# Performance work log

Hardware: AMD Instinct MI355X
Metric: run time of the kernel (lower is better)

The kernel has to match this reference:

```python
import jax, jax.numpy as jnp
import numpy as np

# NSA hyperparams (match init_kwargs)
D_BLK = 64    # d: block stride
L_CMP = 64    # compression block length (== d -> non-overlapping blocks)
L_SLC = 64    # selection block length (== l_cmp == d -> P_slc = P_cmp)
BQ = 64       # block_size_q
TOPK = 16     # slc_top_k
WL, WR = 512, 0  # sliding window (left, right)


def _nsa_forward(q, k, v, w_k, b_k, w_v, b_v, w_gate, b_gate, seqlen):
    S, qh, dim = q.shape
    kv = k.shape[1]
    H = qh // kv
    b = S // seqlen          # number of equal-length packed sequences
    s = seqlen
    scale = dim ** -0.5
    f32 = jnp.float32

    # [b, s, kv, H, e]: q head g*H+h belongs to kv head g (repeat_interleave layout)
    q5 = q.reshape(b, s, kv, H, dim)
    k3 = k.reshape(b, s, kv, dim)
    v3 = v.reshape(b, s, kv, dim)

    # ---- block compression (extract_blocks + cmp_linear over block length) ----
    n_blk = s // D_BLK
    kb = k.reshape(b, n_blk, D_BLK, kv, dim)
    vb = v.reshape(b, n_blk, D_BLK, kv, dim)
    K_cmp = jnp.einsum('bntke,t->bnke', kb, w_k) + b_k[0]
    V_cmp = jnp.einsum('bntke,t->bnke', vb, w_v) + b_v[0]

    # ---- compressed attention (per sequence, fp32 softmax) ----
    sc = jnp.einsum('bqkhe,bnke->bkhqn', q5, K_cmp).astype(f32) * scale
    P = jax.nn.softmax(sc, axis=-1)
    out_cmp = jnp.einsum('bkhqn,bnke->bqkhe', P.astype(q.dtype), V_cmp)

    # ---- selection scores: pool P over q-blocks and GQA groups, then top-k ----
    nqb = s // BQ
    pooled = P.reshape(b, kv, H, nqb, BQ, n_blk).sum(axis=(2, 4))  # [b,kv,nqb,n_blk]
    idx = jax.lax.top_k(pooled, TOPK)[1]                            # [b,kv,nqb,TOPK]

    # gather selected K/V blocks (shared by all queries in a q-block / GQA group)
    kb2 = jnp.transpose(kb, (0, 3, 1, 2, 4))  # [b,kv,n_blk,l,e]
    vb2 = jnp.transpose(vb, (0, 3, 1, 2, 4))
    gather = jax.vmap(jax.vmap(lambda blocks, i: blocks[i]))
    K_sel = gather(kb2, idx)  # [b,kv,nqb,TOPK,l,e]
    V_sel = gather(vb2, idx)

    # ---- selected-block attention ----
    qblk = q5.reshape(b, nqb, BQ, kv, H, dim)
    sc2 = jnp.einsum('bnckhe,bkntle->bkhnctl', qblk, K_sel).astype(f32) * scale
    sc2 = sc2.reshape(b, kv, H, nqb, BQ, TOPK * L_SLC)
    P2 = jax.nn.softmax(sc2, axis=-1).astype(q.dtype)
    out_slc = jnp.einsum('bkhncm,bknme->bnckhe', P2,
                         V_sel.reshape(b, kv, nqb, TOPK * L_SLC, dim))
    out_slc = out_slc.reshape(b, s, kv, H, dim)

    # ---- sliding-window attention (window_size=(WL, WR), non-causal flag) ----
    sw = jnp.einsum('bikhe,bjke->bkhij', q5, k3).astype(f32) * scale
    i = jnp.arange(s)[:, None]
    j = jnp.arange(s)[None, :]
    valid = (j >= i - WL) & (j <= i + WR)
    sw = jnp.where(valid, sw, -jnp.inf)
    Pw = jax.nn.softmax(sw, axis=-1).astype(q.dtype)
    out_win = jnp.einsum('bkhij,bjke->bikhe', Pw, v3)

    # ---- gated fusion of the three branches ----
    gate = jax.nn.sigmoid(jnp.einsum('bqkhe,ec->bqkhc', q5, w_gate) + b_gate)
    out = (gate[..., 0:1] * out_cmp
           + gate[..., 1:2] * out_slc
           + gate[..., 2:3] * out_win)
    return out.reshape(S, qh, dim)


def setup_inputs() -> dict:
    key = jax.random.key(0)
    ks = jax.random.split(key, 9)
    S, qh, kvh, dim = 4096, 8, 2, 128
    inp = {
        'q': jax.random.normal(ks[0], (S, qh, dim), jnp.float32),
        'k': jax.random.normal(ks[1], (S, kvh, dim), jnp.float32),
        'v': jax.random.normal(ks[2], (S, kvh, dim), jnp.float32),
        'w_k': jax.random.normal(ks[3], (L_CMP,), jnp.float32) * (L_CMP ** -0.5),
        'b_k': jax.random.normal(ks[4], (1,), jnp.float32) * 0.02,
        'w_v': jax.random.normal(ks[5], (L_CMP,), jnp.float32) * (L_CMP ** -0.5),
        'b_v': jax.random.normal(ks[6], (1,), jnp.float32) * 0.02,
        'w_gate': jax.random.normal(ks[7], (dim, 3), jnp.float32) * (dim ** -0.5),
        'b_gate': jax.random.normal(ks[8], (3,), jnp.float32) * 0.02,
        'seqlen': 2048,
    }
    return inp


def reference(q, k, v, w_k, b_k, w_v, b_v, w_gate, b_gate, seqlen):
    return _nsa_forward(q, k, v, w_k, b_k, w_v, b_v, w_gate, b_gate, seqlen)
```

## Files before the change

kernel.cpp:

```cpp
#include <hip/hip_runtime.h>
#include <hip/hip_bf16.h>


#define SEQ   2048
#define NB    2
#define KV    2
#define NH    4
#define QH    8
#define DIM   128
#define NBLK  32
#define NQB   32
#define NTOP  16
#define SCALE 0.08838834764831845f
#define QSC   0.12751831795244785f
#define VP    72
#define VCS   40

typedef unsigned short ushort_t;
using bf16x8 = __attribute__((ext_vector_type(8))) short;
using f32x4  = __attribute__((ext_vector_type(4))) float;

__device__ __forceinline__ unsigned pkbf(float a, float b){
  union { __hip_bfloat162 h; unsigned u; } cv;
  cv.h = __float22bfloat162_rn(make_float2(a, b));
  return cv.u;
}
__device__ __forceinline__ ushort_t b16(float f){
  union { float f; unsigned i; } x; x.f = f;
  unsigned r = x.i + 0x7fffu + ((x.i >> 16) & 1u);
  return (ushort_t)(r >> 16);
}
__device__ __forceinline__ float fb(ushort_t h){
  union { unsigned i; float f; } x; x.i = ((unsigned)h) << 16;
  return x.f;
}

__device__ __forceinline__ void async16(ushort_t* l, const ushort_t* g){
  __builtin_amdgcn_global_load_lds(
      (const __attribute__((address_space(1))) unsigned int*)(size_t)g,
      (__attribute__((address_space(3))) unsigned int*)(size_t)l,
      16, 0, 0);
}

__global__ __launch_bounds__(256) void prep_k(
    const float* __restrict__ k, const float* __restrict__ v,
    const float* __restrict__ w_k, const float* __restrict__ b_k,
    const float* __restrict__ w_v, const float* __restrict__ b_v,
    ushort_t* __restrict__ Kb, ushort_t* __restrict__ VT,
    float* __restrict__ Kc, float* __restrict__ Vc)
{
  int blk = blockIdx.x;
  int db = blk & 1, rb = (blk >> 1) & 31, bbg = blk >> 6;
  int bb = bbg >> 1, g = bbg & 1;
  int tid = threadIdx.x;
  __shared__ ushort_t T[64*VP];
  __shared__ float wks[64], wvs[64];
  __shared__ float accK[16][64], accV[16][64];

  if (tid < 64){ wks[tid] = w_k[tid]; wvs[tid] = w_v[tid]; }
  __syncthreads();

  float4 sk = {0,0,0,0}, sv = {0,0,0,0};
  for (int jj = 0; jj < 4; ++jj){
    int i = tid + jj*256;
    int r = i >> 4, ds = i & 15;
    size_t src = ((size_t)(bb*SEQ + rb*64 + r)*KV + g)*DIM + db*64 + ds*4;
    float4 kx = *(const float4*)(k + src);
    float4 vx = *(const float4*)(v + src);
    uint2 kk; kk.x = pkbf(kx.x,kx.y); kk.y = pkbf(kx.z,kx.w);
    size_t rowb = ((size_t)bbg*SEQ + rb*64 + r)*DIM*2;
    int swz = (db*128 + ds*8) ^ ((r & 7) << 4);
    *(uint2*)((char*)Kb + rowb + swz) = kk;
    unsigned v01 = pkbf(vx.x,vx.y), v23 = pkbf(vx.z,vx.w);
    T[(ds*4+0)*VP + r] = (ushort_t)(v01 & 0xffffu);
    T[(ds*4+1)*VP + r] = (ushort_t)(v01 >> 16);
    T[(ds*4+2)*VP + r] = (ushort_t)(v23 & 0xffffu);
    T[(ds*4+3)*VP + r] = (ushort_t)(v23 >> 16);
    float a = wks[r], b = wvs[r];
    sk.x += a*kx.x; sk.y += a*kx.y; sk.z += a*kx.z; sk.w += a*kx.w;
    sv.x += b*vx.x; sv.y += b*vx.y; sv.z += b*vx.z; sv.w += b*vx.w;
  }
  *(float4*)&accK[tid>>4][(tid&15)*4] = sk;
  *(float4*)&accV[tid>>4][(tid&15)*4] = sv;
  __syncthreads();

  for (int jj = 0; jj < 4; ++jj){
    int i = tid + jj*256;
    int d = i >> 4, seg = i & 15;
    uint2 u = *(uint2*)&T[d*VP + seg*4];
    size_t rowb = ((size_t)bbg*DIM + db*64 + d)*SEQ*2;
    int swz = (seg*8) ^ ((d & 7) << 4);
    *(uint2*)((char*)VT + rowb + rb*128 + swz) = u;
  }

  size_t obase = ((size_t)(bbg*NBLK + rb))*DIM + db*64;
  if (tid < 64){
    float s = 0.f;
#pragma unroll
    for (int i = 0; i < 16; ++i) s += accK[i][tid];
    Kc[obase + tid] = s + b_k[0];
  } else if (tid < 128){
    int d = tid - 64;
    float s = 0.f;
#pragma unroll
    for (int i = 0; i < 16; ++i) s += accV[i][d];
    Vc[obase + d] = s + b_v[0];
  }
}

__global__ __launch_bounds__(512, 2) void attn_k(
    const float* __restrict__ q, const ushort_t* __restrict__ Kb,
    const ushort_t* __restrict__ VT,
    const float* __restrict__ Kc, const float* __restrict__ Vc,
    const float* __restrict__ w_gate, const float* __restrict__ b_gate,
    float* __restrict__ slcbuf, float* __restrict__ out)
{
  int idx = blockIdx.x;
  int x = idx & 7, low = idx & 1, u = idx >> 3;
  int bbg = x >> 1;
  int j = u*2 + low;
  int role = j >> 5;
  int qb = j & 31;
  int bb = bbg >> 1, g = bbg & 1;

  int tid = threadIdx.x;
  int lane = tid & 63, w = tid >> 6;
  int quad = lane >> 4, l15 = lane & 15;
  int h = w & 3, qh2 = w >> 2;
  int xr = (l15 & 7) << 4;

  __shared__ ushort_t Ks[2][64*128];
  __shared__ ushort_t VTs[3][128*64];
  __shared__ ushort_t Ps[256*VP];
  __shared__ ushort_t VcTh[128*VCS];
  __shared__ ushort_t VcTl[128*VCS];
  __shared__ float pw[8][NBLK];
  __shared__ float gbuf[256];
  __shared__ int   idxs[NTOP];

  if (role == 0){
    {
      int key = tid >> 4, dq = tid & 15;
      const float* kcs = Kc + ((size_t)bbg*NBLK + key)*DIM + dq*8;
      float4 f0 = *(const float4*)kcs, f1 = *(const float4*)(kcs + 4);
      float fe[8] = {f0.x,f0.y,f0.z,f0.w,f1.x,f1.y,f1.z,f1.w};
      union { ushort_t u[8]; uint4 v; } hi, lo;
#pragma unroll
      for (int e = 0; e < 8; ++e){
        ushort_t hh = b16(fe[e]);
        hi.u[e] = hh; lo.u[e] = b16(fe[e] - fb(hh));
      }
      int off = (dq*16) ^ ((key & 7) << 4);
      *(uint4*)((char*)&Ks[0][0] + key*256 + off) = hi.v;
      *(uint4*)((char*)&Ks[0][0] + (key+32)*256 + off) = lo.v;
    }
    {
      int d = tid & 127, kq = tid >> 7;
      const float* vcs = Vc + (size_t)bbg*NBLK*DIM + d;
      union { ushort_t u[8]; uint4 v; } hi, lo;
#pragma unroll
      for (int kk = 0; kk < 8; ++kk){
        float f = vcs[(kq*8 + kk)*DIM];
        ushort_t hh = b16(f);
        hi.u[kk] = hh; lo.u[kk] = b16(f - fb(hh));
      }
      *(uint4*)&VcTh[d*VCS + kq*8] = hi.v;
      *(uint4*)&VcTl[d*VCS + kq*8] = lo.v;
    }
  }

  const float* qrow0 = q + ((size_t)(bb*SEQ + qb*64 + qh2*32 + l15)*QH + g*NH + h)*DIM;
  const float* qrow1 = qrow0 + (size_t)16*QH*DIM;
  int gcol = 1 + role;
  bf16x8 qfrag0[4], qfrag1[4], qlo0[4], qlo1[4];
  float gp0 = 0.f, gp1 = 0.f, gc0 = 0.f, gc1 = 0.f;
#pragma unroll
  for (int kc = 0; kc < 4; ++kc){
    int d0 = kc*32 + quad*8;
    float4 a0 = *(const float4*)(qrow0 + d0);
    float4 a1 = *(const float4*)(qrow0 + d0 + 4);
    float4 b0 = *(const float4*)(qrow1 + d0);
    float4 b1 = *(const float4*)(qrow1 + d0 + 4);
    float qa[8] = {a0.x,a0.y,a0.z,a0.w,a1.x,a1.y,a1.z,a1.w};
    float qc[8] = {b0.x,b0.y,b0.z,b0.w,b1.x,b1.y,b1.z,b1.w};
#pragma unroll
    for (int jj = 0; jj < 8; ++jj){
      float wg = w_gate[(d0+jj)*3 + gcol];
      gp0 += qa[jj]*wg; gp1 += qc[jj]*wg;
    }
    if (role == 0){
#pragma unroll
      for (int jj = 0; jj < 8; ++jj){
        float w0 = w_gate[(d0+jj)*3];
        gc0 += qa[jj]*w0; gc1 += qc[jj]*w0;
      }
      union { ushort_t u[8]; bf16x8 v; } h0, l0, h1, l1;
#pragma unroll
      for (int e = 0; e < 8; ++e){
        float s0f = qa[e]*QSC; ushort_t hh0 = b16(s0f);
        h0.u[e] = hh0; l0.u[e] = b16(s0f - fb(hh0));
        float s1f = qc[e]*QSC; ushort_t hh1 = b16(s1f);
        h1.u[e] = hh1; l1.u[e] = b16(s1f - fb(hh1));
      }
      qfrag0[kc] = h0.v; qlo0[kc] = l0.v;
      qfrag1[kc] = h1.v; qlo1[kc] = l1.v;
    } else {
      union { unsigned uu[4]; bf16x8 v8; } t0, t1;
#pragma unroll
      for (int p2 = 0; p2 < 4; ++p2){
        t0.uu[p2] = pkbf(qa[2*p2]*QSC, qa[2*p2+1]*QSC);
        t1.uu[p2] = pkbf(qc[2*p2]*QSC, qc[2*p2+1]*QSC);
      }
      qfrag0[kc] = t0.v8; qfrag1[kc] = t1.v8;
    }
  }
  gp0 += __shfl_xor(gp0,16); gp0 += __shfl_xor(gp0,32);
  gp1 += __shfl_xor(gp1,16); gp1 += __shfl_xor(gp1,32);
  if (quad == 0){
    gbuf[w*32 + l15]      = 1.f/(1.f + __expf(-(gp0 + b_gate[gcol])));
    gbuf[w*32 + 16 + l15] = 1.f/(1.f + __expf(-(gp1 + b_gate[gcol])));
  }
  float g0c0 = 0.f, g0c1 = 0.f;
  if (role == 0){
    gc0 += __shfl_xor(gc0,16); gc0 += __shfl_xor(gc0,32);
    gc1 += __shfl_xor(gc1,16); gc1 += __shfl_xor(gc1,32);
    g0c0 = 1.f/(1.f + __expf(-(gc0 + b_gate[0])));
    g0c1 = 1.f/(1.f + __expf(-(gc1 + b_gate[0])));
  }
  __syncthreads();
  float gl0[4], gl1[4];
#pragma unroll
  for (int r = 0; r < 4; ++r){
    gl0[r] = gbuf[w*32 + quad*4 + r];
    gl1[r] = gbuf[w*32 + 16 + quad*4 + r];
  }

  const f32x4 zero4 = {0.f,0.f,0.f,0.f};
  f32x4 cp0[2], cp1[2];
  cp0[0] = zero4; cp0[1] = zero4; cp1[0] = zero4; cp1[1] = zero4;

  if (role == 0){
    f32x4 c0[2], c1[2];
    c0[0]=zero4; c0[1]=zero4; c1[0]=zero4; c1[1]=zero4;
#pragma unroll
    for (int kc = 0; kc < 4; ++kc){
#pragma unroll
      for (int nt = 0; nt < 2; ++nt){
        bf16x8 ah = *(bf16x8*)((char*)&Ks[0][0] + (nt*16 + l15)*256
                               + ((kc*64 + quad*16) ^ xr));
        bf16x8 al = *(bf16x8*)((char*)&Ks[0][0] + (nt*16 + l15 + 32)*256
                               + ((kc*64 + quad*16) ^ xr));
        c0[nt] = __builtin_amdgcn_mfma_f32_16x16x32_bf16(ah, qfrag0[kc], c0[nt], 0, 0, 0);
        c0[nt] = __builtin_amdgcn_mfma_f32_16x16x32_bf16(ah, qlo0[kc],   c0[nt], 0, 0, 0);
        c0[nt] = __builtin_amdgcn_mfma_f32_16x16x32_bf16(al, qfrag0[kc], c0[nt], 0, 0, 0);
        c1[nt] = __builtin_amdgcn_mfma_f32_16x16x32_bf16(ah, qfrag1[kc], c1[nt], 0, 0, 0);
        c1[nt] = __builtin_amdgcn_mfma_f32_16x16x32_bf16(ah, qlo1[kc],   c1[nt], 0, 0, 0);
        c1[nt] = __builtin_amdgcn_mfma_f32_16x16x32_bf16(al, qfrag1[kc], c1[nt], 0, 0, 0);
      }
    }
    float mx0 = -INFINITY, mx1 = -INFINITY;
#pragma unroll
    for (int nt = 0; nt < 2; ++nt)
#pragma unroll
      for (int r = 0; r < 4; ++r){
        mx0 = fmaxf(mx0, c0[nt][r]); mx1 = fmaxf(mx1, c1[nt][r]);
      }
    mx0 = fmaxf(mx0, __shfl_xor(mx0,16)); mx0 = fmaxf(mx0, __shfl_xor(mx0,32));
    mx1 = fmaxf(mx1, __shfl_xor(mx1,16)); mx1 = fmaxf(mx1, __shfl_xor(mx1,32));
    float s0 = 0.f, s1 = 0.f;
#pragma unroll
    for (int nt = 0; nt < 2; ++nt)
#pragma unroll
      for (int r = 0; r < 4; ++r){
        float p0v = exp2f(c0[nt][r] - mx0); c0[nt][r] = p0v; s0 += p0v;
        float p1v = exp2f(c1[nt][r] - mx1); c1[nt][r] = p1v; s1 += p1v;
      }
    s0 += __shfl_xor(s0,16); s0 += __shfl_xor(s0,32);
    s1 += __shfl_xor(s1,16); s1 += __shfl_xor(s1,32);
    float ip0 = 1.f/s0, ip1 = 1.f/s1;
    float ig0 = g0c0*ip0, ig1 = g0c1*ip1;
#pragma unroll
    for (int nt = 0; nt < 2; ++nt)
#pragma unroll
      for (int r = 0; r < 4; ++r){
        cp0[nt][r] = c0[nt][r]*ig0;
        cp1[nt][r] = c1[nt][r]*ig1;
        float t = c0[nt][r]*ip0 + c1[nt][r]*ip1;
        t += __shfl_xor(t,1); t += __shfl_xor(t,2);
        t += __shfl_xor(t,4); t += __shfl_xor(t,8);
        if (l15 == 0) pw[w][nt*16 + quad*4 + r] = t;
      }
    __syncthreads();
    if (tid < 64){
      int n = lane;
      float val = -INFINITY;
      if (n < NBLK){
        float sm = 0.f;
#pragma unroll
        for (int w2 = 0; w2 < 8; ++w2) sm += pw[w2][n];
        val = sm;
      }
      int idxv = n;
      for (int kk = 2; kk <= 32; kk <<= 1){
        for (int jj2 = kk >> 1; jj2 > 0; jj2 >>= 1){
          float pv = __shfl_xor(val, jj2);
          int   pi = __shfl_xor(idxv, jj2);
          bool lower = (lane & jj2) == 0;
          bool desc  = (lane & kk) == 0;
          bool iwin  = (val > pv) || (val == pv && idxv < pi);
          bool keep  = (lower == desc) ? iwin : !iwin;
          if (!keep){ val = pv; idxv = pi; }
        }
      }
      if (lane < NTOP) idxs[lane] = idxv;
    }
    __syncthreads();
  }

  const ushort_t* kbase  = Kb + (size_t)bbg*SEQ*DIM;
  const ushort_t* vtbase = VT + (size_t)bbg*DIM*SEQ;

  int kb0 = (qb >= 8) ? (qb - 8) : 0;
  int nph = (role == 0) ? NTOP : (qb - kb0 + 1);
  int qi0 = qh2*32 + l15, qi1 = qi0 + 16;

  float m10 = -INFINITY, l10 = 0.f, m11 = -INFINITY, l11 = 0.f;
  f32x4 oacc0[8], oacc1[8];
#pragma unroll
  for (int dt = 0; dt < 8; ++dt){ oacc0[dt] = zero4; oacc1[dt] = zero4; }

  auto stage = [&](int kbuf, int vbuf, int kb_){
    const ushort_t* ksrc = kbase + (size_t)kb_*64*DIM;
#pragma unroll
    for (int jj = 0; jj < 2; ++jj)
      async16(&Ks[kbuf][(jj*512 + w*64)*8], ksrc + (size_t)(tid + jj*512)*8);
    const ushort_t* vsrc = vtbase + kb_*64;
#pragma unroll
    for (int jj = 0; jj < 2; ++jj){
      int i = tid + jj*512;
      int d = i >> 3, sg = i & 7;
      async16(&VTs[vbuf][(jj*512 + w*64)*8], vsrc + (size_t)d*SEQ + sg*8);
    }
  };

  stage(0, 0, (role == 0) ? idxs[0] : kb0);

  float alp0 = 1.f, alp1 = 1.f;
  bool  skp0 = true,  skp1 = true;
  int vprev = 2, vcur = 0, vnext = 1;

  for (int t = 0; t < nph; ++t){
    int kb = (role == 0) ? idxs[t] : (kb0 + t);
    __syncthreads();
    if (t+1 < nph){
      int kbn = (role == 0) ? idxs[t+1] : (kb0 + t + 1);
      stage((t+1) & 1, vnext, kbn);
    }
    __builtin_amdgcn_sched_barrier(0);

    f32x4 sacc0[4], sacc1[4];
#pragma unroll
    for (int nt = 0; nt < 4; ++nt){ sacc0[nt] = zero4; sacc1[nt] = zero4; }
    __builtin_amdgcn_s_setprio(1);
#pragma unroll
    for (int kc = 0; kc < 4; ++kc){
#pragma unroll
      for (int nt = 0; nt < 4; ++nt){
        bf16x8 a = *(bf16x8*)((char*)&Ks[t & 1][0] + (nt*16 + l15)*256
                              + ((kc*64 + quad*16) ^ xr));
        sacc0[nt] = __builtin_amdgcn_mfma_f32_16x16x32_bf16(a, qfrag0[kc], sacc0[nt], 0, 0, 0);
        sacc1[nt] = __builtin_amdgcn_mfma_f32_16x16x32_bf16(a, qfrag1[kc], sacc1[nt], 0, 0, 0);
      }
    }
    __builtin_amdgcn_s_setprio(0);

    if (t > 0){
      if (!skp0){
        float ar[4];
#pragma unroll
        for (int r = 0; r < 4; ++r) ar[r] = __shfl(alp0, quad*4 + r);
#pragma unroll
        for (int dt = 0; dt < 8; ++dt)
#pragma unroll
          for (int r = 0; r < 4; ++r) oacc0[dt][r] *= ar[r];
      }
      if (!skp1){
        float ar[4];
#pragma unroll
        for (int r = 0; r < 4; ++r) ar[r] = __shfl(alp1, quad*4 + r);
#pragma unroll
        for (int dt = 0; dt < 8; ++dt)
#pragma unroll
          for (int r = 0; r < 4; ++r) oacc1[dt][r] *= ar[r];
      }
#pragma unroll
      for (int kc2 = 0; kc2 < 2; ++kc2){
        bf16x8 pa0 = *(bf16x8*)&Ps[(w*32 + l15)*VP + kc2*32 + quad*8];
        bf16x8 pa1 = *(bf16x8*)&Ps[(w*32 + 16 + l15)*VP + kc2*32 + quad*8];
        __builtin_amdgcn_s_setprio(1);
#pragma unroll
        for (int dt = 0; dt < 8; ++dt){
          bf16x8 vb8 = *(bf16x8*)((char*)&VTs[vprev][0] + (dt*16 + l15)*128
                                  + ((kc2*64 + quad*16) ^ xr));
          oacc0[dt] = __builtin_amdgcn_mfma_f32_16x16x32_bf16(pa0, vb8, oacc0[dt], 0, 0, 0);
          oacc1[dt] = __builtin_amdgcn_mfma_f32_16x16x32_bf16(pa1, vb8, oacc1[dt], 0, 0, 0);
        }
        __builtin_amdgcn_s_setprio(0);
      }
    }

    bool mlow  = (role == 1) && (kb == qb - 8);
    bool mhigh = (role == 1) && (kb == qb);
    bool domask = mlow | mhigh;

    auto softmax_qt = [&](f32x4* sc2, float& m1r, float& l1r, int qi_l,
                          bool& skipped) -> float {
      if (domask){
#pragma unroll
        for (int nt = 0; nt < 4; ++nt)
#pragma unroll
          for (int r = 0; r < 4; ++r){
            int key = nt*16 + quad*4 + r;
            bool valid = (!mlow || key >= qi_l) && (!mhigh || key <= qi_l);
            sc2[nt][r] = valid ? sc2[nt][r] : -INFINITY;
          }
      }
      float mnt[4];
#pragma unroll
      for (int nt = 0; nt < 4; ++nt)
        mnt[nt] = fmaxf(fmaxf(sc2[nt][0], sc2[nt][1]),
                        fmaxf(sc2[nt][2], sc2[nt][3]));
      float mx = fmaxf(fmaxf(mnt[0], mnt[1]), fmaxf(mnt[2], mnt[3]));
      mx = fmaxf(mx, __shfl_xor(mx, 16));
      mx = fmaxf(mx, __shfl_xor(mx, 32));
      float al = 1.f;
      skipped = __all(mx <= m1r + 8.f);
      if (!skipped){
        float mn = fmaxf(m1r, mx);
        al = exp2f(m1r - mn);
        m1r = mn;
      }
      float snt[4];
#pragma unroll
      for (int nt = 0; nt < 4; ++nt){
        float p0 = exp2f(sc2[nt][0] - m1r);
        float p1 = exp2f(sc2[nt][1] - m1r);
        float p2 = exp2f(sc2[nt][2] - m1r);
        float p3 = exp2f(sc2[nt][3] - m1r);
        sc2[nt][0] = p0; sc2[nt][1] = p1; sc2[nt][2] = p2; sc2[nt][3] = p3;
        snt[nt] = (p0 + p1) + (p2 + p3);
      }
      float s0 = (snt[0] + snt[1]) + (snt[2] + snt[3]);
      s0 += __shfl_xor(s0, 16);
      s0 += __shfl_xor(s0, 32);
      l1r = l1r*al + s0;
      return al;
    };
    bool sk0, sk1;
    float al0 = softmax_qt(sacc0, m10, l10, qi0, sk0);
    float al1 = softmax_qt(sacc1, m11, l11, qi1, sk1);
    alp0 = al0; skp0 = sk0;
    alp1 = al1; skp1 = sk1;

#pragma unroll
    for (int nt = 0; nt < 4; ++nt){
      uint2 p0, p1;
      p0.x = pkbf(sacc0[nt][0], sacc0[nt][1]);
      p0.y = pkbf(sacc0[nt][2], sacc0[nt][3]);
      p1.x = pkbf(sacc1[nt][0], sacc1[nt][1]);
      p1.y = pkbf(sacc1[nt][2], sacc1[nt][3]);
      *(uint2*)&Ps[(w*32 + l15)*VP + nt*16 + quad*4] = p0;
      *(uint2*)&Ps[(w*32 + 16 + l15)*VP + nt*16 + quad*4] = p1;
    }

    int tmpv = vprev; vprev = vcur; vcur = vnext; vnext = tmpv;
  }

  {
    if (!skp0){
      float ar[4];
#pragma unroll
      for (int r = 0; r < 4; ++r) ar[r] = __shfl(alp0, quad*4 + r);
#pragma unroll
      for (int dt = 0; dt < 8; ++dt)
#pragma unroll
        for (int r = 0; r < 4; ++r) oacc0[dt][r] *= ar[r];
    }
    if (!skp1){
      float ar[4];
#pragma unroll
      for (int r = 0; r < 4; ++r) ar[r] = __shfl(alp1, quad*4 + r);
#pragma unroll
      for (int dt = 0; dt < 8; ++dt)
#pragma unroll
        for (int r = 0; r < 4; ++r) oacc1[dt][r] *= ar[r];
    }
#pragma unroll
    for (int kc2 = 0; kc2 < 2; ++kc2){
      bf16x8 pa0 = *(bf16x8*)&Ps[(w*32 + l15)*VP + kc2*32 + quad*8];
      bf16x8 pa1 = *(bf16x8*)&Ps[(w*32 + 16 + l15)*VP + kc2*32 + quad*8];
#pragma unroll
      for (int dt = 0; dt < 8; ++dt){
        bf16x8 vb8 = *(bf16x8*)((char*)&VTs[vprev][0] + (dt*16 + l15)*128
                                + ((kc2*64 + quad*16) ^ xr));
        oacc0[dt] = __builtin_amdgcn_mfma_f32_16x16x32_bf16(pa0, vb8, oacc0[dt], 0, 0, 0);
        oacc1[dt] = __builtin_amdgcn_mfma_f32_16x16x32_bf16(pa1, vb8, oacc1[dt], 0, 0, 0);
      }
    }
  }

  float lr0[4], lr1[4];
#pragma unroll
  for (int r = 0; r < 4; ++r){
    lr0[r] = __shfl(l10, quad*4 + r);
    lr1[r] = __shfl(l11, quad*4 + r);
  }
  if (role == 0){
    float a0[4], a1[4];
#pragma unroll
    for (int r = 0; r < 4; ++r){ a0[r] = gl0[r]/lr0[r]; a1[r] = gl1[r]/lr1[r]; }
#pragma unroll
    for (int dt = 0; dt < 8; ++dt)
#pragma unroll
      for (int r = 0; r < 4; ++r){ oacc0[dt][r] *= a0[r]; oacc1[dt][r] *= a1[r]; }
#pragma unroll
    for (int nt = 0; nt < 2; ++nt){
      union { ushort_t u[4]; uint2 v; } h0, l0, h1, l1;
#pragma unroll
      for (int r = 0; r < 4; ++r){
        ushort_t hh0 = b16(cp0[nt][r]);
        h0.u[r] = hh0; l0.u[r] = b16(cp0[nt][r] - fb(hh0));
        ushort_t hh1 = b16(cp1[nt][r]);
        h1.u[r] = hh1; l1.u[r] = b16(cp1[nt][r] - fb(hh1));
      }
      *(uint2*)&Ps[(w*32 + l15)*VP + nt*16 + quad*4]      = h0.v;
      *(uint2*)&Ps[(w*32 + l15)*VP + 32 + nt*16 + quad*4] = l0.v;
      *(uint2*)&Ps[(w*32 + 16 + l15)*VP + nt*16 + quad*4]      = h1.v;
      *(uint2*)&Ps[(w*32 + 16 + l15)*VP + 32 + nt*16 + quad*4] = l1.v;
    }
    bf16x8 pah0 = *(bf16x8*)&Ps[(w*32 + l15)*VP + quad*8];
    bf16x8 pal0 = *(bf16x8*)&Ps[(w*32 + l15)*VP + 32 + quad*8];
    bf16x8 pah1 = *(bf16x8*)&Ps[(w*32 + 16 + l15)*VP + quad*8];
    bf16x8 pal1 = *(bf16x8*)&Ps[(w*32 + 16 + l15)*VP + 32 + quad*8];
#pragma unroll
    for (int dt = 0; dt < 8; ++dt){
      bf16x8 vbh = *(bf16x8*)&VcTh[(dt*16 + l15)*VCS + quad*8];
      bf16x8 vbl = *(bf16x8*)&VcTl[(dt*16 + l15)*VCS + quad*8];
      oacc0[dt] = __builtin_amdgcn_mfma_f32_16x16x32_bf16(pah0, vbh, oacc0[dt], 0, 0, 0);
      oacc0[dt] = __builtin_amdgcn_mfma_f32_16x16x32_bf16(pah0, vbl, oacc0[dt], 0, 0, 0);
      oacc0[dt] = __builtin_amdgcn_mfma_f32_16x16x32_bf16(pal0, vbh, oacc0[dt], 0, 0, 0);
      oacc1[dt] = __builtin_amdgcn_mfma_f32_16x16x32_bf16(pah1, vbh, oacc1[dt], 0, 0, 0);
      oacc1[dt] = __builtin_amdgcn_mfma_f32_16x16x32_bf16(pah1, vbl, oacc1[dt], 0, 0, 0);
      oacc1[dt] = __builtin_amdgcn_mfma_f32_16x16x32_bf16(pal1, vbh, oacc1[dt], 0, 0, 0);
    }
#pragma unroll
    for (int r = 0; r < 4; ++r){
      size_t ob0 = ((size_t)(bb*SEQ + qb*64 + qh2*32 + quad*4 + r)*QH + g*NH + h)*DIM + l15;
      size_t ob1 = ob0 + (size_t)16*QH*DIM;
      float* op0 = slcbuf + ob0;
      float* op1 = slcbuf + ob1;
#pragma unroll
      for (int dt = 0; dt < 8; ++dt){
        op0[dt*16] = oacc0[dt][r];
        op1[dt*16] = oacc1[dt][r];
      }
    }
  } else {
#pragma unroll
    for (int r = 0; r < 4; ++r){
      float s20 = gl0[r] / lr0[r];
      float s21 = gl1[r] / lr1[r];
      size_t ob0 = ((size_t)(bb*SEQ + qb*64 + qh2*32 + quad*4 + r)*QH + g*NH + h)*DIM + l15;
      size_t ob1 = ob0 + (size_t)16*QH*DIM;
      float* op0 = out + ob0;
      float* op1 = out + ob1;
#pragma unroll
      for (int dt = 0; dt < 8; ++dt){
        op0[dt*16] = s20 * oacc0[dt][r];
        op1[dt*16] = s21 * oacc1[dt][r];
      }
    }
  }
}

__global__ __launch_bounds__(256) void merge_k(const float* __restrict__ slcbuf,
                                               float* __restrict__ out){
  int i = blockIdx.x * 256 + threadIdx.x;
  float4 a = ((const float4*)slcbuf)[i];
  float4 b = ((float4*)out)[i];
  b.x += a.x; b.y += a.y; b.z += a.z; b.w += a.w;
  ((float4*)out)[i] = b;
}

extern "C" void kernel_launch(void* const* d_in, const int* in_sizes, int n_in,
                              void* d_out, int out_size, void* d_ws, size_t ws_size,
                              hipStream_t stream) {
  const float* q      = (const float*)d_in[0];
  const float* k      = (const float*)d_in[1];
  const float* v      = (const float*)d_in[2];
  const float* w_k    = (const float*)d_in[3];
  const float* b_k    = (const float*)d_in[4];
  const float* w_v    = (const float*)d_in[5];
  const float* b_v    = (const float*)d_in[6];
  const float* w_gate = (const float*)d_in[7];
  const float* b_gate = (const float*)d_in[8];
  float* out = (float*)d_out;

  float* ws     = (float*)d_ws;
  float* Kc     = ws;
  float* Vc     = ws + 16384;
  float* slcbuf = ws + 49152;
  ushort_t* Kb  = (ushort_t*)(ws + 4243456);
  ushort_t* VT  = Kb + 1048576;

  prep_k <<<256, 256, 0, stream>>>(k, v, w_k, b_k, w_v, b_v, Kb, VT, Kc, Vc);
  attn_k <<<256, 512, 0, stream>>>(q, Kb, VT, Kc, Vc, w_gate, b_gate, slcbuf, out);
  merge_k<<<4096, 256, 0, stream>>>(slcbuf, out);
}
```

Measured before the change: 162.9 us.

## Split KV range across two blocks per tile with split-softmax merge

Doubles the attn grid so each selection and sliding-window tile is handled by two blocks, each covering half of the KV blocks. Partial outputs go out unnormalized along with per-row max and sum, and the merge kernel combines them flash-decoding style. The compressed-attention P·V product moves out of the attention kernel into the merge kernel as an fp32 loop over 32 compressed values. Async LDS double/triple buffering is replaced by register-staged single-buffer loads with extra barriers, which shrinks LDS so occupancy can rise to 4 blocks per CU. The cost is more global traffic through the new device buffers and less overlap of loads with compute.

```diff
diff --git a/kernel.cpp b/kernel.cpp
--- a/kernel.cpp
+++ b/kernel.cpp
@@ -14,11 +14,16 @@
 #define SCALE 0.08838834764831845f
 #define QSC   0.12751831795244785f
 #define VP    72
-#define VCS   40
+#define VSU   68
 
 typedef unsigned short ushort_t;
 using bf16x8 = __attribute__((ext_vector_type(8))) short;
 using f32x4  = __attribute__((ext_vector_type(4))) float;
+
+__device__ float g_slcB[4194304];
+__device__ float g_winB[4194304];
+__device__ float g_cp[1048576];
+__device__ float g_mlg[4][65536];
 
 __device__ __forceinline__ unsigned pkbf(float a, float b){
   union { __hip_bfloat162 h; unsigned u; } cv;
@@ -33,13 +38,6 @@
 __device__ __forceinline__ float fb(ushort_t h){
   union { unsigned i; float f; } x; x.i = ((unsigned)h) << 16;
   return x.f;
-}
-
-__device__ __forceinline__ void async16(ushort_t* l, const ushort_t* g){
-  __builtin_amdgcn_global_load_lds(
-      (const __attribute__((address_space(1))) unsigned int*)(size_t)g,
-      (__attribute__((address_space(3))) unsigned int*)(size_t)l,
-      16, 0, 0);
 }
 
 __global__ __launch_bounds__(256) void prep_k(
@@ -108,10 +106,9 @@
   }
 }
 
-__global__ __launch_bounds__(512, 2) void attn_k(
+__global__ __launch_bounds__(512, 4) void attn_k(
     const float* __restrict__ q, const ushort_t* __restrict__ Kb,
-    const ushort_t* __restrict__ VT,
-    const float* __restrict__ Kc, const float* __restrict__ Vc,
+    const ushort_t* __restrict__ VT, const float* __restrict__ Kc,
     const float* __restrict__ w_gate, const float* __restrict__ b_gate,
     float* __restrict__ slcbuf, float* __restrict__ out)
 {
@@ -119,7 +116,8 @@
   int x = idx & 7, low = idx & 1, u = idx >> 3;
   int bbg = x >> 1;
   int j = u*2 + low;
-  int role = j >> 5;
+  int role = j >> 6;
+  int sub  = (j >> 5) & 1;
   int qb = j & 31;
   int bb = bbg >> 1, g = bbg & 1;
 
@@ -129,44 +127,27 @@
   int h = w & 3, qh2 = w >> 2;
   int xr = (l15 & 7) << 4;
 
-  __shared__ ushort_t Ks[2][64*128];
-  __shared__ ushort_t VTs[3][128*64];
+  __shared__ ushort_t Ks[64*128];
+  __shared__ ushort_t Vs[128*VSU];
   __shared__ ushort_t Ps[256*VP];
-  __shared__ ushort_t VcTh[128*VCS];
-  __shared__ ushort_t VcTl[128*VCS];
   __shared__ float pw[8][NBLK];
   __shared__ float gbuf[256];
   __shared__ int   idxs[NTOP];
 
   if (role == 0){
-    {
-      int key = tid >> 4, dq = tid & 15;
-      const float* kcs = Kc + ((size_t)bbg*NBLK + key)*DIM + dq*8;
-      float4 f0 = *(const float4*)kcs, f1 = *(const float4*)(kcs + 4);
-      float fe[8] = {f0.x,f0.y,f0.z,f0.w,f1.x,f1.y,f1.z,f1.w};
-      union { ushort_t u[8]; uint4 v; } hi, lo;
-#pragma unroll
-      for (int e = 0; e < 8; ++e){
-        ushort_t hh = b16(fe[e]);
-        hi.u[e] = hh; lo.u[e] = b16(fe[e] - fb(hh));
-      }
-      int off = (dq*16) ^ ((key & 7) << 4);
-      *(uint4*)((char*)&Ks[0][0] + key*256 + off) = hi.v;
-      *(uint4*)((char*)&Ks[0][0] + (key+32)*256 + off) = lo.v;
-    }
-    {
-      int d = tid & 127, kq = tid >> 7;
-      const float* vcs = Vc + (size_t)bbg*NBLK*DIM + d;
-      union { ushort_t u[8]; uint4 v; } hi, lo;
-#pragma unroll
-      for (int kk = 0; kk < 8; ++kk){
-        float f = vcs[(kq*8 + kk)*DIM];
-        ushort_t hh = b16(f);
-        hi.u[kk] = hh; lo.u[kk] = b16(f - fb(hh));
-      }
-      *(uint4*)&VcTh[d*VCS + kq*8] = hi.v;
-      *(uint4*)&VcTl[d*VCS + kq*8] = lo.v;
-    }
+    int key = tid >> 4, dq = tid & 15;
+    const float* kcs = Kc + ((size_t)bbg*NBLK + key)*DIM + dq*8;
+    float4 f0 = *(const float4*)kcs, f1 = *(const float4*)(kcs + 4);
+    float fe[8] = {f0.x,f0.y,f0.z,f0.w,f1.x,f1.y,f1.z,f1.w};
+    union { ushort_t u[8]; uint4 v; } hi, lo;
+#pragma unroll
+    for (int e = 0; e < 8; ++e){
+      ushort_t hh = b16(fe[e]);
+      hi.u[e] = hh; lo.u[e] = b16(fe[e] - fb(hh));
+    }
+    int off = (dq*16) ^ ((key & 7) << 4);
+    *(uint4*)((char*)&Ks[0] + key*256 + off) = hi.v;
+    *(uint4*)((char*)&Ks[0] + (key+32)*256 + off) = lo.v;
   }
 
   const float* qrow0 = q + ((size_t)(bb*SEQ + qb*64 + qh2*32 + l15)*QH + g*NH + h)*DIM;
@@ -236,8 +217,6 @@
   }
 
   const f32x4 zero4 = {0.f,0.f,0.f,0.f};
-  f32x4 cp0[2], cp1[2];
-  cp0[0] = zero4; cp0[1] = zero4; cp1[0] = zero4; cp1[1] = zero4;
 
   if (role == 0){
     f32x4 c0[2], c1[2];
@@ -246,9 +225,9 @@
     for (int kc = 0; kc < 4; ++kc){
 #pragma unroll
       for (int nt = 0; nt < 2; ++nt){
-        bf16x8 ah = *(bf16x8*)((char*)&Ks[0][0] + (nt*16 + l15)*256
+        bf16x8 ah = *(bf16x8*)((char*)&Ks[0] + (nt*16 + l15)*256
                                + ((kc*64 + quad*16) ^ xr));
-        bf16x8 al = *(bf16x8*)((char*)&Ks[0][0] + (nt*16 + l15 + 32)*256
+        bf16x8 al = *(bf16x8*)((char*)&Ks[0] + (nt*16 + l15 + 32)*256
                                + ((kc*64 + quad*16) ^ xr));
         c0[nt] = __builtin_amdgcn_mfma_f32_16x16x32_bf16(ah, qfrag0[kc], c0[nt], 0, 0, 0);
         c0[nt] = __builtin_amdgcn_mfma_f32_16x16x32_bf16(ah, qlo0[kc],   c0[nt], 0, 0, 0);
@@ -278,13 +257,23 @@
     s0 += __shfl_xor(s0,16); s0 += __shfl_xor(s0,32);
     s1 += __shfl_xor(s1,16); s1 += __shfl_xor(s1,32);
     float ip0 = 1.f/s0, ip1 = 1.f/s1;
-    float ig0 = g0c0*ip0, ig1 = g0c1*ip1;
+    if (sub == 0){
+      float ig0 = g0c0*ip0, ig1 = g0c1*ip1;
+      size_t rh0 = ((size_t)(bb*SEQ + qb*64 + qh2*32 + l15)*QH + g*NH + h);
+      size_t rh1 = rh0 + (size_t)16*QH;
+#pragma unroll
+      for (int nt = 0; nt < 2; ++nt)
+#pragma unroll
+        for (int r = 0; r < 4; ++r){
+          int key = nt*16 + quad*4 + r;
+          g_cp[rh0*NBLK + key] = c0[nt][r]*ig0;
+          g_cp[rh1*NBLK + key] = c1[nt][r]*ig1;
+        }
+    }
 #pragma unroll
     for (int nt = 0; nt < 2; ++nt)
 #pragma unroll
       for (int r = 0; r < 4; ++r){
-        cp0[nt][r] = c0[nt][r]*ig0;
-        cp1[nt][r] = c1[nt][r]*ig1;
         float t = c0[nt][r]*ip0 + c1[nt][r]*ip1;
         t += __shfl_xor(t,1); t += __shfl_xor(t,2);
         t += __shfl_xor(t,4); t += __shfl_xor(t,8);
@@ -321,7 +310,10 @@
   const ushort_t* vtbase = VT + (size_t)bbg*DIM*SEQ;
 
   int kb0 = (qb >= 8) ? (qb - 8) : 0;
-  int nph = (role == 0) ? NTOP : (qb - kb0 + 1);
+  int N   = qb - kb0 + 1;
+  int nph0 = (N + 1) >> 1;
+  int nph = (role == 0) ? 8 : (sub ? (N - nph0) : nph0);
+  int tb  = kb0 + sub*nph0;
   int qi0 = qh2*32 + l15, qi1 = qi0 + 16;
 
   float m10 = -INFINITY, l10 = 0.f, m11 = -INFINITY, l11 = 0.f;
@@ -329,70 +321,139 @@
 #pragma unroll
   for (int dt = 0; dt < 8; ++dt){ oacc0[dt] = zero4; oacc1[dt] = zero4; }
 
-  auto stage = [&](int kbuf, int vbuf, int kb_){
-    const ushort_t* ksrc = kbase + (size_t)kb_*64*DIM;
-#pragma unroll
-    for (int jj = 0; jj < 2; ++jj)
-      async16(&Ks[kbuf][(jj*512 + w*64)*8], ksrc + (size_t)(tid + jj*512)*8);
-    const ushort_t* vsrc = vtbase + kb_*64;
-#pragma unroll
-    for (int jj = 0; jj < 2; ++jj){
-      int i = tid + jj*512;
-      int d = i >> 3, sg = i & 7;
-      async16(&VTs[vbuf][(jj*512 + w*64)*8], vsrc + (size_t)d*SEQ + sg*8);
+  uint2 kr[4], vr[4];
+  auto loadKV = [&](int rowbase){
+#pragma unroll
+    for (int jj = 0; jj < 4; ++jj){
+      int unit = tid + jj*512;
+      int krow = unit >> 5, kseg = unit & 31;
+      kr[jj] = *(const uint2*)(kbase + (size_t)(rowbase + krow)*DIM + kseg*4);
+      int vd = unit >> 4, vsg = unit & 15;
+      vr[jj] = *(const uint2*)(vtbase + (size_t)vd*SEQ + rowbase + vsg*4);
     }
   };
-
-  stage(0, 0, (role == 0) ? idxs[0] : kb0);
-
-  float alp0 = 1.f, alp1 = 1.f;
-  bool  skp0 = true,  skp1 = true;
-  int vprev = 2, vcur = 0, vnext = 1;
-
-  for (int t = 0; t < nph; ++t){
-    int kb = (role == 0) ? idxs[t] : (kb0 + t);
+  auto writeKV = [&](){
+#pragma unroll
+    for (int jj = 0; jj < 4; ++jj){
+      int unit = tid + jj*512;
+      int krow = unit >> 5, kseg = unit & 31;
+      *(uint2*)&Ks[krow*128 + kseg*4] = kr[jj];
+      int vd = unit >> 4, vsg = unit & 15;
+      *(uint2*)&Vs[vd*VSU + vsg*4] = vr[jj];
+    }
+  };
+
+  if (nph > 0){
+    int r0 = (role == 0) ? idxs[sub*8]*64 : tb*64;
+    loadKV(r0);
+    writeKV();
     __syncthreads();
-    if (t+1 < nph){
-      int kbn = (role == 0) ? idxs[t+1] : (kb0 + t + 1);
-      stage((t+1) & 1, vnext, kbn);
-    }
-    __builtin_amdgcn_sched_barrier(0);
-
-    f32x4 sacc0[4], sacc1[4];
-#pragma unroll
-    for (int nt = 0; nt < 4; ++nt){ sacc0[nt] = zero4; sacc1[nt] = zero4; }
-    __builtin_amdgcn_s_setprio(1);
-#pragma unroll
-    for (int kc = 0; kc < 4; ++kc){
+
+    for (int t = 0; t < nph; ++t){
+      int kb = (role == 0) ? idxs[sub*8 + t] : (tb + t);
+      if (t+1 < nph){
+        int rn = (role == 0) ? idxs[sub*8 + t + 1]*64 : (tb + t + 1)*64;
+        loadKV(rn);
+      }
+      __builtin_amdgcn_sched_barrier(0);
+
+      f32x4 sacc0[4], sacc1[4];
+#pragma unroll
+      for (int nt = 0; nt < 4; ++nt){ sacc0[nt] = zero4; sacc1[nt] = zero4; }
+      __builtin_amdgcn_s_setprio(1);
+#pragma unroll
+      for (int kc = 0; kc < 4; ++kc){
+#pragma unroll
+        for (int nt = 0; nt < 4; ++nt){
+          bf16x8 a = *(bf16x8*)((char*)&Ks[0] + (nt*16 + l15)*256
+                                + ((kc*64 + quad*16) ^ xr));
+          sacc0[nt] = __builtin_amdgcn_mfma_f32_16x16x32_bf16(a, qfrag0[kc], sacc0[nt], 0, 0, 0);
+          sacc1[nt] = __builtin_amdgcn_mfma_f32_16x16x32_bf16(a, qfrag1[kc], sacc1[nt], 0, 0, 0);
+        }
+      }
+      __builtin_amdgcn_s_setprio(0);
+
+      bool mlow  = (role == 1) && (qb >= 8) && (kb == qb - 8);
+      bool mhigh = (role == 1) && (kb == qb);
+      bool domask = mlow | mhigh;
+
+      auto softmax_qt = [&](f32x4* sc2, float& m1r, float& l1r, int qi_l,
+                            bool& skipped) -> float {
+        if (domask){
+#pragma unroll
+          for (int nt = 0; nt < 4; ++nt)
+#pragma unroll
+            for (int r = 0; r < 4; ++r){
+              int key = nt*16 + quad*4 + r;
+              bool valid = (!mlow || key >= qi_l) && (!mhigh || key <= qi_l);
+              sc2[nt][r] = valid ? sc2[nt][r] : -INFINITY;
+            }
+        }
+        float mnt[4];
+#pragma unroll
+        for (int nt = 0; nt < 4; ++nt)
+          mnt[nt] = fmaxf(fmaxf(sc2[nt][0], sc2[nt][1]),
+                          fmaxf(sc2[nt][2], sc2[nt][3]));
+        float mx = fmaxf(fmaxf(mnt[0], mnt[1]), fmaxf(mnt[2], mnt[3]));
+        mx = fmaxf(mx, __shfl_xor(mx, 16));
+        mx = fmaxf(mx, __shfl_xor(mx, 32));
+        float al = 1.f;
+        skipped = __all(mx <= m1r + 8.f);
+        if (!skipped){
+          float mn = fmaxf(m1r, mx);
+          al = exp2f(m1r - mn);
+          m1r = mn;
+        }
+        float snt[4];
+#pragma unroll
+        for (int nt = 0; nt < 4; ++nt){
+          float p0 = exp2f(sc2[nt][0] - m1r);
+          float p1 = exp2f(sc2[nt][1] - m1r);
+          float p2 = exp2f(sc2[nt][2] - m1r);
+          float p3 = exp2f(sc2[nt][3] - m1r);
+          sc2[nt][0] = p0; sc2[nt][1] = p1; sc2[nt][2] = p2; sc2[nt][3] = p3;
+          snt[nt] = (p0 + p1) + (p2 + p3);
+        }
+        float s0 = (snt[0] + snt[1]) + (snt[2] + snt[3]);
+        s0 += __shfl_xor(s0, 16);
+        s0 += __shfl_xor(s0, 32);
+        l1r = l1r*al + s0;
+        return al;
+      };
+      bool sk0, sk1;
+      float al0 = softmax_qt(sacc0, m10, l10, qi0, sk0);
+      float al1 = softmax_qt(sacc1, m11, l11, qi1, sk1);
+
 #pragma unroll
       for (int nt = 0; nt < 4; ++nt){
-        bf16x8 a = *(bf16x8*)((char*)&Ks[t & 1][0] + (nt*16 + l15)*256
-                              + ((kc*64 + quad*16) ^ xr));
-        sacc0[nt] = __builtin_amdgcn_mfma_f32_16x16x32_bf16(a, qfrag0[kc], sacc0[nt], 0, 0, 0);
-        sacc1[nt] = __builtin_amdgcn_mfma_f32_16x16x32_bf16(a, qfrag1[kc], sacc1[nt], 0, 0, 0);
-      }
-    }
-    __builtin_amdgcn_s_setprio(0);
-
-    if (t > 0){
-      if (!skp0){
+        uint2 p0, p1;
+        p0.x = pkbf(sacc0[nt][0], sacc0[nt][1]);
+        p0.y = pkbf(sacc0[nt][2], sacc0[nt][3]);
+        p1.x = pkbf(sacc1[nt][0], sacc1[nt][1]);
+        p1.y = pkbf(sacc1[nt][2], sacc1[nt][3]);
+        *(uint2*)&Ps[(w*32 + l15)*VP + nt*16 + quad*4] = p0;
+        *(uint2*)&Ps[(w*32 + 16 + l15)*VP + nt*16 + quad*4] = p1;
+      }
+
+      if (!sk0){
         float ar[4];
 #pragma unroll
-        for (int r = 0; r < 4; ++r) ar[r] = __shfl(alp0, quad*4 + r);
+        for (int r = 0; r < 4; ++r) ar[r] = __shfl(al0, quad*4 + r);
 #pragma unroll
         for (int dt = 0; dt < 8; ++dt)
 #pragma unroll
           for (int r = 0; r < 4; ++r) oacc0[dt][r] *= ar[r];
       }
-      if (!skp1){
+      if (!sk1){
         float ar[4];
 #pragma unroll
-        for (int r = 0; r < 4; ++r) ar[r] = __shfl(alp1, quad*4 + r);
+        for (int r = 0; r < 4; ++r) ar[r] = __shfl(al1, quad*4 + r);
 #pragma unroll
         for (int dt = 0; dt < 8; ++dt)
 #pragma unroll
           for (int r = 0; r < 4; ++r) oacc1[dt][r] *= ar[r];
       }
+
 #pragma unroll
       for (int kc2 = 0; kc2 < 2; ++kc2){
         bf16x8 pa0 = *(bf16x8*)&Ps[(w*32 + l15)*VP + kc2*32 + quad*8];
@@ -400,196 +461,94 @@
         __builtin_amdgcn_s_setprio(1);
 #pragma unroll
         for (int dt = 0; dt < 8; ++dt){
-          bf16x8 vb8 = *(bf16x8*)((char*)&VTs[vprev][0] + (dt*16 + l15)*128
+          bf16x8 vb8 = *(bf16x8*)((char*)&Vs[0] + (dt*16 + l15)*(VSU*2)
                                   + ((kc2*64 + quad*16) ^ xr));
           oacc0[dt] = __builtin_amdgcn_mfma_f32_16x16x32_bf16(pa0, vb8, oacc0[dt], 0, 0, 0);
           oacc1[dt] = __builtin_amdgcn_mfma_f32_16x16x32_bf16(pa1, vb8, oacc1[dt], 0, 0, 0);
         }
         __builtin_amdgcn_s_setprio(0);
       }
-    }
-
-    bool mlow  = (role == 1) && (kb == qb - 8);
-    bool mhigh = (role == 1) && (kb == qb);
-    bool domask = mlow | mhigh;
-
-    auto softmax_qt = [&](f32x4* sc2, float& m1r, float& l1r, int qi_l,
-                          bool& skipped) -> float {
-      if (domask){
-#pragma unroll
-        for (int nt = 0; nt < 4; ++nt)
-#pragma unroll
-          for (int r = 0; r < 4; ++r){
-            int key = nt*16 + quad*4 + r;
-            bool valid = (!mlow || key >= qi_l) && (!mhigh || key <= qi_l);
-            sc2[nt][r] = valid ? sc2[nt][r] : -INFINITY;
-          }
-      }
-      float mnt[4];
-#pragma unroll
-      for (int nt = 0; nt < 4; ++nt)
-        mnt[nt] = fmaxf(fmaxf(sc2[nt][0], sc2[nt][1]),
-                        fmaxf(sc2[nt][2], sc2[nt][3]));
-      float mx = fmaxf(fmaxf(mnt[0], mnt[1]), fmaxf(mnt[2], mnt[3]));
-      mx = fmaxf(mx, __shfl_xor(mx, 16));
-      mx = fmaxf(mx, __shfl_xor(mx, 32));
-      float al = 1.f;
-      skipped = __all(mx <= m1r + 8.f);
-      if (!skipped){
-        float mn = fmaxf(m1r, mx);
-        al = exp2f(m1r - mn);
-        m1r = mn;
-      }
-      float snt[4];
-#pragma unroll
-      for (int nt = 0; nt < 4; ++nt){
-        float p0 = exp2f(sc2[nt][0] - m1r);
-        float p1 = exp2f(sc2[nt][1] - m1r);
-        float p2 = exp2f(sc2[nt][2] - m1r);
-        float p3 = exp2f(sc2[nt][3] - m1r);
-        sc2[nt][0] = p0; sc2[nt][1] = p1; sc2[nt][2] = p2; sc2[nt][3] = p3;
-        snt[nt] = (p0 + p1) + (p2 + p3);
-      }
-      float s0 = (snt[0] + snt[1]) + (snt[2] + snt[3]);
-      s0 += __shfl_xor(s0, 16);
-      s0 += __shfl_xor(s0, 32);
-      l1r = l1r*al + s0;
-      return al;
-    };
-    bool sk0, sk1;
-    float al0 = softmax_qt(sacc0, m10, l10, qi0, sk0);
-    float al1 = softmax_qt(sacc1, m11, l11, qi1, sk1);
-    alp0 = al0; skp0 = sk0;
-    alp1 = al1; skp1 = sk1;
-
-#pragma unroll
-    for (int nt = 0; nt < 4; ++nt){
-      uint2 p0, p1;
-      p0.x = pkbf(sacc0[nt][0], sacc0[nt][1]);
-      p0.y = pkbf(sacc0[nt][2], sacc0[nt][3]);
-      p1.x = pkbf(sacc1[nt][0], sacc1[nt][1]);
-      p1.y = pkbf(sacc1[nt][2], sacc1[nt][3]);
-      *(uint2*)&Ps[(w*32 + l15)*VP + nt*16 + quad*4] = p0;
-      *(uint2*)&Ps[(w*32 + 16 + l15)*VP + nt*16 + quad*4] = p1;
-    }
-
-    int tmpv = vprev; vprev = vcur; vcur = vnext; vnext = tmpv;
-  }
-
-  {
-    if (!skp0){
-      float ar[4];
-#pragma unroll
-      for (int r = 0; r < 4; ++r) ar[r] = __shfl(alp0, quad*4 + r);
-#pragma unroll
-      for (int dt = 0; dt < 8; ++dt)
-#pragma unroll
-        for (int r = 0; r < 4; ++r) oacc0[dt][r] *= ar[r];
-    }
-    if (!skp1){
-      float ar[4];
-#pragma unroll
-      for (int r = 0; r < 4; ++r) ar[r] = __shfl(alp1, quad*4 + r);
-#pragma unroll
-      for (int dt = 0; dt < 8; ++dt)
-#pragma unroll
-        for (int r = 0; r < 4; ++r) oacc1[dt][r] *= ar[r];
-    }
-#pragma unroll
-    for (int kc2 = 0; kc2 < 2; ++kc2){
-      bf16x8 pa0 = *(bf16x8*)&Ps[(w*32 + l15)*VP + kc2*32 + quad*8];
-      bf16x8 pa1 = *(bf16x8*)&Ps[(w*32 + 16 + l15)*VP + kc2*32 + quad*8];
-#pragma unroll
-      for (int dt = 0; dt < 8; ++dt){
-        bf16x8 vb8 = *(bf16x8*)((char*)&VTs[vprev][0] + (dt*16 + l15)*128
-                                + ((kc2*64 + quad*16) ^ xr));
-        oacc0[dt] = __builtin_amdgcn_mfma_f32_16x16x32_bf16(pa0, vb8, oacc0[dt], 0, 0, 0);
-        oacc1[dt] = __builtin_amdgcn_mfma_f32_16x16x32_bf16(pa1, vb8, oacc1[dt], 0, 0, 0);
-      }
-    }
-  }
-
-  float lr0[4], lr1[4];
+
+      if (t+1 < nph){
+        __syncthreads();
+        writeKV();
+        __syncthreads();
+      }
+    }
+  }
+
+  int stream = role*2 + sub;
+  float* obuf = (role == 0) ? (sub ? g_slcB : slcbuf)
+                            : (sub ? g_winB : out);
 #pragma unroll
   for (int r = 0; r < 4; ++r){
-    lr0[r] = __shfl(l10, quad*4 + r);
-    lr1[r] = __shfl(l11, quad*4 + r);
-  }
-  if (role == 0){
-    float a0[4], a1[4];
-#pragma unroll
-    for (int r = 0; r < 4; ++r){ a0[r] = gl0[r]/lr0[r]; a1[r] = gl1[r]/lr1[r]; }
-#pragma unroll
-    for (int dt = 0; dt < 8; ++dt)
-#pragma unroll
-      for (int r = 0; r < 4; ++r){ oacc0[dt][r] *= a0[r]; oacc1[dt][r] *= a1[r]; }
-#pragma unroll
-    for (int nt = 0; nt < 2; ++nt){
-      union { ushort_t u[4]; uint2 v; } h0, l0, h1, l1;
-#pragma unroll
-      for (int r = 0; r < 4; ++r){
-        ushort_t hh0 = b16(cp0[nt][r]);
-        h0.u[r] = hh0; l0.u[r] = b16(cp0[nt][r] - fb(hh0));
-        ushort_t hh1 = b16(cp1[nt][r]);
-        h1.u[r] = hh1; l1.u[r] = b16(cp1[nt][r] - fb(hh1));
-      }
-      *(uint2*)&Ps[(w*32 + l15)*VP + nt*16 + quad*4]      = h0.v;
-      *(uint2*)&Ps[(w*32 + l15)*VP + 32 + nt*16 + quad*4] = l0.v;
-      *(uint2*)&Ps[(w*32 + 16 + l15)*VP + nt*16 + quad*4]      = h1.v;
-      *(uint2*)&Ps[(w*32 + 16 + l15)*VP + 32 + nt*16 + quad*4] = l1.v;
-    }
-    bf16x8 pah0 = *(bf16x8*)&Ps[(w*32 + l15)*VP + quad*8];
-    bf16x8 pal0 = *(bf16x8*)&Ps[(w*32 + l15)*VP + 32 + quad*8];
-    bf16x8 pah1 = *(bf16x8*)&Ps[(w*32 + 16 + l15)*VP + quad*8];
-    bf16x8 pal1 = *(bf16x8*)&Ps[(w*32 + 16 + l15)*VP + 32 + quad*8];
+    float s20 = gl0[r];
+    float s21 = gl1[r];
+    size_t ob0 = ((size_t)(bb*SEQ + qb*64 + qh2*32 + quad*4 + r)*QH + g*NH + h)*DIM + l15;
+    size_t ob1 = ob0 + (size_t)16*QH*DIM;
+    float* op0 = obuf + ob0;
+    float* op1 = obuf + ob1;
 #pragma unroll
     for (int dt = 0; dt < 8; ++dt){
-      bf16x8 vbh = *(bf16x8*)&VcTh[(dt*16 + l15)*VCS + quad*8];
-      bf16x8 vbl = *(bf16x8*)&VcTl[(dt*16 + l15)*VCS + quad*8];
-      oacc0[dt] = __builtin_amdgcn_mfma_f32_16x16x32_bf16(pah0, vbh, oacc0[dt], 0, 0, 0);
-      oacc0[dt] = __builtin_amdgcn_mfma_f32_16x16x32_bf16(pah0, vbl, oacc0[dt], 0, 0, 0);
-      oacc0[dt] = __builtin_amdgcn_mfma_f32_16x16x32_bf16(pal0, vbh, oacc0[dt], 0, 0, 0);
-      oacc1[dt] = __builtin_amdgcn_mfma_f32_16x16x32_bf16(pah1, vbh, oacc1[dt], 0, 0, 0);
-      oacc1[dt] = __builtin_amdgcn_mfma_f32_16x16x32_bf16(pah1, vbl, oacc1[dt], 0, 0, 0);
-      oacc1[dt] = __builtin_amdgcn_mfma_f32_16x16x32_bf16(pal1, vbh, oacc1[dt], 0, 0, 0);
-    }
-#pragma unroll
-    for (int r = 0; r < 4; ++r){
-      size_t ob0 = ((size_t)(bb*SEQ + qb*64 + qh2*32 + quad*4 + r)*QH + g*NH + h)*DIM + l15;
-      size_t ob1 = ob0 + (size_t)16*QH*DIM;
-      float* op0 = slcbuf + ob0;
-      float* op1 = slcbuf + ob1;
-#pragma unroll
-      for (int dt = 0; dt < 8; ++dt){
-        op0[dt*16] = oacc0[dt][r];
-        op1[dt*16] = oacc1[dt][r];
-      }
-    }
-  } else {
-#pragma unroll
-    for (int r = 0; r < 4; ++r){
-      float s20 = gl0[r] / lr0[r];
-      float s21 = gl1[r] / lr1[r];
-      size_t ob0 = ((size_t)(bb*SEQ + qb*64 + qh2*32 + quad*4 + r)*QH + g*NH + h)*DIM + l15;
-      size_t ob1 = ob0 + (size_t)16*QH*DIM;
-      float* op0 = out + ob0;
-      float* op1 = out + ob1;
-#pragma unroll
-      for (int dt = 0; dt < 8; ++dt){
-        op0[dt*16] = s20 * oacc0[dt][r];
-        op1[dt*16] = s21 * oacc1[dt][r];
-      }
-    }
-  }
-}
-
-__global__ __launch_bounds__(256) void merge_k(const float* __restrict__ slcbuf,
-                                               float* __restrict__ out){
+      op0[dt*16] = s20 * oacc0[dt][r];
+      op1[dt*16] = s21 * oacc1[dt][r];
+    }
+  }
+  if (quad == 0){
+    size_t rh0 = ((size_t)(bb*SEQ + qb*64 + qh2*32 + l15)*QH + g*NH + h);
+    size_t rh1 = rh0 + (size_t)16*QH;
+    g_mlg[stream][rh0*2]     = m10;
+    g_mlg[stream][rh0*2 + 1] = l10;
+    g_mlg[stream][rh1*2]     = m11;
+    g_mlg[stream][rh1*2 + 1] = l11;
+  }
+}
+
+__global__ __launch_bounds__(256) void merge_k(
+    const float* __restrict__ slcA, const float* __restrict__ Vc,
+    float* __restrict__ out)
+{
   int i = blockIdx.x * 256 + threadIdx.x;
-  float4 a = ((const float4*)slcbuf)[i];
-  float4 b = ((float4*)out)[i];
-  b.x += a.x; b.y += a.y; b.z += a.z; b.w += a.w;
-  ((float4*)out)[i] = b;
+  int rh = i >> 5;
+  int d4 = (i & 31) * 4;
+
+  float mA = g_mlg[0][rh*2], lA = g_mlg[0][rh*2+1];
+  float mB = g_mlg[1][rh*2], lB = g_mlg[1][rh*2+1];
+  float Ms = fmaxf(mA, mB);
+  float wA = exp2f(mA - Ms), wB = exp2f(mB - Ms);
+  float isl = 1.f/(lA*wA + lB*wB);
+  float4 a4 = ((const float4*)slcA)[i];
+  float4 b4 = ((const float4*)g_slcB)[i];
+  float ox = (a4.x*wA + b4.x*wB)*isl;
+  float oy = (a4.y*wA + b4.y*wB)*isl;
+  float oz = (a4.z*wA + b4.z*wB)*isl;
+  float ow = (a4.w*wA + b4.w*wB)*isl;
+
+  float mC = g_mlg[2][rh*2], lC = g_mlg[2][rh*2+1];
+  float mD = g_mlg[3][rh*2], lD = g_mlg[3][rh*2+1];
+  float Mw = fmaxf(mC, mD);
+  float wC = exp2f(mC - Mw), wD = exp2f(mD - Mw);
+  float isw = 1.f/(lC*wC + lD*wD);
+  float4 c4 = ((const float4*)out)[i];
+  float4 e4 = ((const float4*)g_winB)[i];
+  ox += (c4.x*wC + e4.x*wD)*isw;
+  oy += (c4.y*wC + e4.y*wD)*isw;
+  oz += (c4.z*wC + e4.z*wD)*isw;
+  ow += (c4.w*wC + e4.w*wD)*isw;
+
+  int row = rh >> 3, head = rh & 7;
+  int bbg = (row >> 11)*2 + (head >> 2);
+  const float* vc = Vc + ((size_t)bbg*NBLK)*DIM + d4;
+  const float* cp = g_cp + (size_t)rh*NBLK;
+  float cx = 0.f, cy = 0.f, cz = 0.f, cw = 0.f;
+#pragma unroll 8
+  for (int n = 0; n < NBLK; ++n){
+    float p = cp[n];
+    float4 v4 = *(const float4*)(vc + (size_t)n*DIM);
+    cx += p*v4.x; cy += p*v4.y; cz += p*v4.z; cw += p*v4.w;
+  }
+  float4 o; o.x = ox + cx; o.y = oy + cy; o.z = oz + cz; o.w = ow + cw;
+  ((float4*)out)[i] = o;
 }
 
 extern "C" void kernel_launch(void* const* d_in, const int* in_sizes, int n_in,
@@ -614,6 +573,6 @@
   ushort_t* VT  = Kb + 1048576;
 
   prep_k <<<256, 256, 0, stream>>>(k, v, w_k, b_k, w_v, b_v, Kb, VT, Kc, Vc);
-  attn_k <<<256, 512, 0, stream>>>(q, Kb, VT, Kc, Vc, w_gate, b_gate, slcbuf, out);
-  merge_k<<<4096, 256, 0, stream>>>(slcbuf, out);
-}
+  attn_k <<<512, 512, 0, stream>>>(q, Kb, VT, Kc, w_gate, b_gate, slcbuf, out);
+  merge_k<<<4096, 256, 0, stream>>>(slcbuf, Vc, out);
+}
```

Result: slower. 301.4 us (+85.1%).
